# Kernel tuning notes

Hardware: AMD Instinct MI355X
Metric: run time of the kernel (lower is better)

## Reference

```python
import jax, jax.numpy as jnp
from jax import lax
import numpy as np

KAPPA_S = 6.0
KAPPA_D = 5.0
POLICY_STRETCH = 2.0
VALUE_STRETCH = 1.0 / 32.0
VALUE_GAUGE = 0.2

RAW_PATTERNS = [
    [[0, 0, 0, 0, -5, 1, 1, 1, 1], [0, 0, 0, 0, -5, -5, -5, -5, -5], 0],
    [[0, 0, 0, 1, -5, 1, 1, 1, 0], [0, 0, 0, -5, -5, -5, -5, -5, 0], 0],
    [[0, 0, 1, 1, -5, 1, 1, 0, 0], [0, 0, -5, -5, -5, -5, -5, 0, 0], 0],
    [[0, 1, 1, 1, -5, 1, 0, 0, 0], [0, -5, -5, -5, -5, -5, 0, 0, 0], 0],
    [[1, 1, 1, 1, -5, 0, 0, 0, 0], [-5, -5, -5, -5, -5, 0, 0, 0, 0], 0],
    [[0, -5, 1, 1, 1, 1, 1, -5, 0], [0, 0, -5, -5, -5, -5, -5, 0, 0], -4],
]


def _all_3xnxn(p3):
    # Lay a 9-long 1D pattern (one per input channel) along the 4 line
    # directions (horizontal, vertical, two diagonals) of a 9x9 kernel.
    f = np.zeros((9, 9, 3, 4), np.float32)
    for ch in range(3):
        v = np.asarray(p3[ch], np.float32)
        f[4, :, ch, 0] = v                       # horizontal
        f[:, 4, ch, 1] = v                       # vertical
        for i in range(9):
            f[i, i, ch, 2] = v[i]                # main diagonal
            f[i, 8 - i, ch, 3] = v[i]            # anti diagonal
    return f


def _assemble_filters():
    # select_patterns: channel 0 -> [offense, defense, defense]; channel 1 -> [defense, offense, defense]
    patterns = []
    for off, de, bias in RAW_PATTERNS:
        patterns.append(([off, de, de], bias))
        patterns.append(([de, off, de], bias))
    filt = np.stack([_all_3xnxn(p) for p, _ in patterns], axis=3)  # (9,9,3,12,4)
    filt = np.reshape(filt, (9, 9, 3, -1))                          # filter idx = 4*pattern + direction
    biases = np.asarray([b for _, b in patterns for _ in range(4)], np.float32)
    return jnp.asarray(filt), jnp.asarray(biases)


def _safe_pow(x, p):
    # x >= 0 everywhere it is used; guards the grad of x**p (p<1) at x==0.
    pos = x > 0
    return jnp.where(pos, jnp.where(pos, x, 1.0) ** p, 0.0)


def setup_inputs() -> dict:
    key = jax.random.key(0)
    state = jax.random.normal(key, (4096, 19, 19, 3), dtype=jnp.float32)
    W, b = _assemble_filters()
    return {"state": state, "W": W, "b": b}


def reference(state, W, b):
    # detector: Conv2D 9x9, 48 filters, SAME padding, relu
    counts = jax.nn.relu(
        lax.conv_general_dilated(
            state, W, window_strides=(1, 1), padding="SAME",
            dimension_numbers=("NHWC", "HWIO", "NHWC"),
        ) + b
    )  # [B, N, N, 48]
    # peel: 3x3 conv with identity-center kernel, VALID padding == crop of 1
    core = counts[:, 1:-1, 1:-1, :]  # [B, N-2, N-2, 48]
    B, H, Wd, _ = core.shape
    # filter index = 8*shift + 4*channel + direction for the 40 line filters
    core40 = core[..., :40].reshape(B, H, Wd, 5, 2, 4)  # (shift, channel, direction)
    s = jnp.sum(core40 ** KAPPA_S, axis=3)               # sum over shifts -> [B,H,W,2,4]
    sd = jnp.sum(_safe_pow(s, KAPPA_D / KAPPA_S), axis=4)  # sum over directions -> [B,H,W,2]
    f = _safe_pow(sd, 1.0 / KAPPA_D)                     # [B,H,W,2]; [...,c] = field(channel c)
    f_cur, f_oth = f[..., 0], f[..., 1]
    logits = (f_cur + f_oth).reshape(B, -1)
    probs = jax.nn.softmax(POLICY_STRETCH * logits, axis=-1)
    raw_value = VALUE_GAUGE * (jnp.sum(f_cur, axis=(1, 2)) - jnp.sum(f_oth, axis=(1, 2)))
    value = jnp.tanh(VALUE_STRETCH * raw_value)
    return probs, value
```

## Files before the change

kernel.cpp:

```cpp
#include <hip/hip_runtime.h>
#include <math.h>


__device__ __forceinline__ float fpow(float x, float e) {
    float r = __builtin_amdgcn_exp2f(e * __builtin_amdgcn_logf(x));
    return (x > 0.f) ? r : 0.f;
}
__device__ __forceinline__ float fexp(float x) {
    return __builtin_amdgcn_exp2f(x * 1.44269504088896f);
}

#define OFF_E0 0
#define OFF_E1 729
#define OFF_C0 1458
#define OFF_C1 1747
#define OFF_GH 2036
#define OFF_GV 2750
#define OFF_GD 3464
#define OFF_GA 4916
#define DUMMY  6302
#define LDS_FLOATS 6303

__global__ __launch_bounds__(320) void topo_policy_value(
    const float* __restrict__ state,
    float* __restrict__ probs,
    float* __restrict__ value)
{
    __shared__ float lds[LDS_FLOATS];
    __shared__ float red[16];

    const int tid = threadIdx.x;
    const int b = blockIdx.x;

    #pragma unroll
    for (int i = 0; i < 5; ++i) {
        int idx = tid + i * 320;
        if (idx < 1458) lds[idx] = 0.0f;
    }
    __syncthreads();

    const float* src = state + (size_t)b * (19 * 19 * 3);
    for (int j = tid; j < 361; j += 320) {
        int br = j / 19, bc = j - br * 19;
        float l0 = src[3 * j], l1 = src[3 * j + 1], l2 = src[3 * j + 2];
        float e0 = fmaf(-5.f, l1 + l2, l0);
        float e1 = fmaf(-5.f, l0 + l2, l1);
        int pi = (br + 4) * 27 + (bc + 4);
        lds[OFF_E0 + pi] = e0;
        lds[OFF_E1 + pi] = e1;
        if (br >= 1 && br <= 17 && bc >= 1 && bc <= 17) {
            int ci = (br - 1) * 17 + (bc - 1);
            lds[OFF_C0 + ci] = 6.f * l0;
            lds[OFF_C1 + ci] = 6.f * l1;
        }
    }
    __syncthreads();

    if (tid < 200) {
        int t = tid, f, L;
        int base, step, outp, cnt;
        if (t < 34) {
            f = t & 1; L = t >> 1;
            base = (L + 5) * 27 + 1; step = 1;
            outp = OFF_GH + f * 357 + L * 21; cnt = 21;
        } else if (t < 68) {
            t -= 34; f = t & 1; L = t >> 1;
            base = 27 + (L + 5); step = 27;
            outp = OFF_GV + f * 357 + L * 21; cnt = 21;
        } else if (t < 134) {
            t -= 68; f = t & 1; L = t >> 1;
            int d = L - 16;
            int j0 = (d < 0) ? -d : 0;
            base = (j0 + 1 + d) * 27 + (j0 + 1); step = 28;
            outp = OFF_GD + f * 726 + L * 22 + j0;
            cnt = 21 - ((d < 0) ? -d : d);
        } else {
            t -= 134; f = t & 1; L = t >> 1;
            int k0 = (L > 16) ? (L - 16) : 0;
            int k1 = (L + 4 < 20) ? (L + 4) : 20;
            base = 26 * k0 + 36 + L; step = 26;
            outp = OFF_GA + f * 693 + L * 21 + k0;
            cnt = k1 - k0 + 1;
        }
        const float* ef = lds + (f ? OFF_E1 : OFF_E0);
        float s = ef[base] + ef[base + step] + ef[base + 2 * step]
                + ef[base + 3 * step] + ef[base + 4 * step];
        #pragma unroll
        for (int i = 0; i < 21; ++i) {
            int dst = (i < cnt) ? (outp + i) : DUMMY;
            lds[dst] = s;
            s += ef[base + (i + 5) * step] - ef[base + i * step];
        }
    }
    __syncthreads();

    const bool act = tid < 289;
    float fcur = 0.f, foth = 0.f;
    if (act) {
        const int y = tid / 17;
        const int x = tid - y * 17;
        const float h0 = lds[OFF_C0 + tid];
        const float h1 = lds[OFF_C1 + tid];

        const int bh = OFF_GH + y * 21 + x;
        const int bv = OFF_GV + x * 21 + y;
        const int bd = OFF_GD + (y - x + 16) * 22 + x;
        const int ba = OFF_GA + (y + x) * 21 + y;

        float sd0 = 0.f, sd1 = 0.f;
        #define ORIENT(B, FS)                                         \
        {                                                             \
            float t0 = 0.f, t1 = 0.f;                                 \
            _Pragma("unroll")                                         \
            for (int i = 0; i < 5; ++i) {                             \
                float a0 = lds[(B) + i] - h0;                         \
                float a1 = lds[(B) + (FS) + i] - h1;                  \
                a0 = fmaxf(a0, 0.f); a1 = fmaxf(a1, 0.f);             \
                float q0 = a0 * a0, q1 = a1 * a1;                     \
                float m0 = q0 * q0, m1 = q1 * q1;                     \
                t0 = fmaf(m0, q0, t0); t1 = fmaf(m1, q1, t1);         \
            }                                                         \
            sd0 += fpow(t0, 5.0f / 6.0f);                             \
            sd1 += fpow(t1, 5.0f / 6.0f);                             \
        }
        ORIENT(bh, 357)
        ORIENT(bv, 357)
        ORIENT(bd, 726)
        ORIENT(ba, 693)
        #undef ORIENT

        fcur = fpow(sd0, 0.2f);
        foth = fpow(sd1, 0.2f);
    }

    const float g = act ? 2.f * (fcur + foth) : -3.0e38f;
    float lmax = g;
    float ldif = fcur - foth;

    #pragma unroll
    for (int off = 32; off > 0; off >>= 1) {
        lmax = fmaxf(lmax, __shfl_down(lmax, off, 64));
        ldif += __shfl_down(ldif, off, 64);
    }
    const int wave = tid >> 6;
    if ((tid & 63) == 0) { red[wave] = lmax; red[5 + wave] = ldif; }
    __syncthreads();
    if (tid == 0) {
        float m = red[0];
        #pragma unroll
        for (int w = 1; w < 5; ++w) m = fmaxf(m, red[w]);
        red[15] = m;
        red[14] = red[5] + red[6] + red[7] + red[8] + red[9];
    }
    __syncthreads();

    const float M = red[15];
    const float e = act ? fexp(g - M) : 0.f;
    float lsum = e;
    #pragma unroll
    for (int off = 32; off > 0; off >>= 1) lsum += __shfl_down(lsum, off, 64);
    if ((tid & 63) == 0) red[wave] = lsum;
    __syncthreads();
    if (tid == 0) red[13] = red[0] + red[1] + red[2] + red[3] + red[4];
    __syncthreads();

    const float invS = 1.0f / red[13];
    if (act) probs[(size_t)b * 289 + tid] = e * invS;
    if (tid == 0) value[b] = tanhf(red[14] * (0.2f / 32.0f));
}

extern "C" void kernel_launch(void* const* d_in, const int* in_sizes, int n_in,
                              void* d_out, int out_size, void* d_ws, size_t ws_size,
                              hipStream_t stream) {
    const float* state = (const float*)d_in[0];
    const int nb = in_sizes[0] / (19 * 19 * 3);
    float* probs = (float*)d_out;
    float* value = probs + (size_t)nb * 289;
    topo_policy_value<<<dim3(nb), dim3(320), 0, stream>>>(state, probs, value);
}
```

Baseline: 88.33 us.

## Interleave both channels as float2 in LDS and cache sliding window in registers

After: 85.27 us. -3.5%, faster.

```diff
diff --git a/kernel.cpp b/kernel.cpp
--- a/kernel.cpp
+++ b/kernel.cpp
@@ -10,86 +10,86 @@
     return __builtin_amdgcn_exp2f(x * 1.44269504088896f);
 }
 
-#define OFF_E0 0
-#define OFF_E1 729
-#define OFF_C0 1458
-#define OFF_C1 1747
-#define OFF_GH 2036
-#define OFF_GV 2750
-#define OFF_GD 3464
-#define OFF_GA 4916
-#define DUMMY  6302
-#define LDS_FLOATS 6303
+#define F2_E   0
+#define F2_C   729
+#define F2_GH  1018
+#define F2_GV  1375
+#define F2_GD  1732
+#define F2_GA  2458
+#define F2_DUMMY 3151
+#define F2_TOTAL 3152
 
 __global__ __launch_bounds__(320) void topo_policy_value(
     const float* __restrict__ state,
     float* __restrict__ probs,
     float* __restrict__ value)
 {
-    __shared__ float lds[LDS_FLOATS];
+    __shared__ float2 l2[F2_TOTAL];
     __shared__ float red[16];
 
     const int tid = threadIdx.x;
     const int b = blockIdx.x;
 
     #pragma unroll
-    for (int i = 0; i < 5; ++i) {
+    for (int i = 0; i < 3; ++i) {
         int idx = tid + i * 320;
-        if (idx < 1458) lds[idx] = 0.0f;
+        if (idx < 729) l2[idx] = make_float2(0.f, 0.f);
     }
     __syncthreads();
 
     const float* src = state + (size_t)b * (19 * 19 * 3);
     for (int j = tid; j < 361; j += 320) {
         int br = j / 19, bc = j - br * 19;
-        float l0 = src[3 * j], l1 = src[3 * j + 1], l2 = src[3 * j + 2];
-        float e0 = fmaf(-5.f, l1 + l2, l0);
-        float e1 = fmaf(-5.f, l0 + l2, l1);
-        int pi = (br + 4) * 27 + (bc + 4);
-        lds[OFF_E0 + pi] = e0;
-        lds[OFF_E1 + pi] = e1;
+        float l0 = src[3 * j], l1 = src[3 * j + 1], l2v = src[3 * j + 2];
+        float e0 = fmaf(-5.f, l1 + l2v, l0);
+        float e1 = fmaf(-5.f, l0 + l2v, l1);
+        l2[F2_E + (br + 4) * 27 + (bc + 4)] = make_float2(e0, e1);
         if (br >= 1 && br <= 17 && bc >= 1 && bc <= 17) {
-            int ci = (br - 1) * 17 + (bc - 1);
-            lds[OFF_C0 + ci] = 6.f * l0;
-            lds[OFF_C1 + ci] = 6.f * l1;
+            l2[F2_C + (br - 1) * 17 + (bc - 1)] = make_float2(6.f * l0, 6.f * l1);
         }
     }
     __syncthreads();
 
-    if (tid < 200) {
-        int t = tid, f, L;
+    if (tid < 100) {
+        int t = tid, L;
         int base, step, outp, cnt;
-        if (t < 34) {
-            f = t & 1; L = t >> 1;
+        if (t < 17) {
+            L = t;
             base = (L + 5) * 27 + 1; step = 1;
-            outp = OFF_GH + f * 357 + L * 21; cnt = 21;
-        } else if (t < 68) {
-            t -= 34; f = t & 1; L = t >> 1;
+            outp = F2_GH + L * 21; cnt = 21;
+        } else if (t < 34) {
+            L = t - 17;
             base = 27 + (L + 5); step = 27;
-            outp = OFF_GV + f * 357 + L * 21; cnt = 21;
-        } else if (t < 134) {
-            t -= 68; f = t & 1; L = t >> 1;
+            outp = F2_GV + L * 21; cnt = 21;
+        } else if (t < 67) {
+            L = t - 34;
             int d = L - 16;
             int j0 = (d < 0) ? -d : 0;
             base = (j0 + 1 + d) * 27 + (j0 + 1); step = 28;
-            outp = OFF_GD + f * 726 + L * 22 + j0;
+            outp = F2_GD + L * 22 + j0;
             cnt = 21 - ((d < 0) ? -d : d);
         } else {
-            t -= 134; f = t & 1; L = t >> 1;
+            L = t - 67;
             int k0 = (L > 16) ? (L - 16) : 0;
             int k1 = (L + 4 < 20) ? (L + 4) : 20;
             base = 26 * k0 + 36 + L; step = 26;
-            outp = OFF_GA + f * 693 + L * 21 + k0;
+            outp = F2_GA + L * 21 + k0;
             cnt = k1 - k0 + 1;
         }
-        const float* ef = lds + (f ? OFF_E1 : OFF_E0);
-        float s = ef[base] + ef[base + step] + ef[base + 2 * step]
-                + ef[base + 3 * step] + ef[base + 4 * step];
+        float2 buf[5];
+        #pragma unroll
+        for (int i = 0; i < 5; ++i) buf[i] = l2[base + i * step];
+        float sx = buf[0].x + buf[1].x + buf[2].x + buf[3].x + buf[4].x;
+        float sy = buf[0].y + buf[1].y + buf[2].y + buf[3].y + buf[4].y;
         #pragma unroll
         for (int i = 0; i < 21; ++i) {
-            int dst = (i < cnt) ? (outp + i) : DUMMY;
-            lds[dst] = s;
-            s += ef[base + (i + 5) * step] - ef[base + i * step];
+            int dst = (i < cnt) ? (outp + i) : F2_DUMMY;
+            l2[dst] = make_float2(sx, sy);
+            float2 nc = l2[base + (i + 5) * step];
+            float2 oc = buf[i % 5];
+            sx += nc.x - oc.x;
+            sy += nc.y - oc.y;
+            buf[i % 5] = nc;
         }
     }
     __syncthreads();
@@ -99,23 +99,22 @@
     if (act) {
         const int y = tid / 17;
         const int x = tid - y * 17;
-        const float h0 = lds[OFF_C0 + tid];
-        const float h1 = lds[OFF_C1 + tid];
+        const float2 h = l2[F2_C + tid];
 
-        const int bh = OFF_GH + y * 21 + x;
-        const int bv = OFF_GV + x * 21 + y;
-        const int bd = OFF_GD + (y - x + 16) * 22 + x;
-        const int ba = OFF_GA + (y + x) * 21 + y;
+        const int bh = F2_GH + y * 21 + x;
+        const int bv = F2_GV + x * 21 + y;
+        const int bd = F2_GD + (y - x + 16) * 22 + x;
+        const int ba = F2_GA + (y + x) * 21 + y;
 
         float sd0 = 0.f, sd1 = 0.f;
-        #define ORIENT(B, FS)                                         \
+        #define ORIENT(B)                                             \
         {                                                             \
             float t0 = 0.f, t1 = 0.f;                                 \
             _Pragma("unroll")                                         \
             for (int i = 0; i < 5; ++i) {                             \
-                float a0 = lds[(B) + i] - h0;                         \
-                float a1 = lds[(B) + (FS) + i] - h1;                  \
-                a0 = fmaxf(a0, 0.f); a1 = fmaxf(a1, 0.f);             \
+                float2 w = l2[(B) + i];                               \
+                float a0 = fmaxf(w.x - h.x, 0.f);                     \
+                float a1 = fmaxf(w.y - h.y, 0.f);                     \
                 float q0 = a0 * a0, q1 = a1 * a1;                     \
                 float m0 = q0 * q0, m1 = q1 * q1;                     \
                 t0 = fmaf(m0, q0, t0); t1 = fmaf(m1, q1, t1);         \
@@ -123,10 +122,10 @@
             sd0 += fpow(t0, 5.0f / 6.0f);                             \
             sd1 += fpow(t1, 5.0f / 6.0f);                             \
         }
-        ORIENT(bh, 357)
-        ORIENT(bv, 357)
-        ORIENT(bd, 726)
-        ORIENT(ba, 693)
+        ORIENT(bh)
+        ORIENT(bv)
+        ORIENT(bd)
+        ORIENT(ba)
         #undef ORIENT
 
         fcur = fpow(sd0, 0.2f);
```
